# Performance work log

Hardware: AMD Instinct MI355X
Metric: run time of the kernel (lower is better)

Reference implementation:

```python
import jax, jax.numpy as jnp
import numpy as np

INF = 1e20


def setup_inputs() -> dict:
    key = jax.random.key(0)
    k1, k2, k3 = jax.random.split(key, 3)
    B, Q, M, F, D = 16, 64, 512, 16, 512
    return {
        "query_embed": jax.random.normal(k1, (B, Q, D), dtype=jnp.float32),
        "in_memory_embed": jax.random.normal(k2, (B, M, F, D), dtype=jnp.float32),
        "out_memory_embed": jax.random.normal(k3, (B, M, F, D), dtype=jnp.float32),
        "ctx_mask": jnp.ones((B, M, F), dtype=jnp.float32),
        "query_mask": jnp.ones((B, Q), dtype=jnp.float32),
    }


def reference(query_embed, in_memory_embed, out_memory_embed, ctx_mask, query_mask):
    # co-attention scores: [B, Q, M, F]
    attention = jnp.einsum("bqd,bmfd->bqmf", query_embed, in_memory_embed)
    # additive INF masking (torch: mask*att - (1-mask)*INF)
    cm = ctx_mask[:, None, :, :]            # [B,1,M,F]
    attention = cm * attention - (1.0 - cm) * INF
    qm = query_mask[:, :, None, None]       # [B,Q,1,1]
    attention = qm * attention - (1.0 - qm) * INF
    # NOTE: torch code computes a max-pool over Q for kb_feature_att but
    # immediately overwrites it with softmax of a ones/ctx mask -> dead code.
    mask = ctx_mask * 1.0 - (1.0 - ctx_mask) * INF        # [B,M,F]
    kb_feature_att = jax.nn.softmax(mask, axis=-1)        # [B,M,F]
    # weighted read over feature slots: [B,M,D]
    in_mem = jnp.einsum("bmf,bmfd->bmd", kb_feature_att, in_memory_embed)
    out_mem = out_memory_embed.sum(axis=2)                # [B,M,D]
    # max-pool over feature axis F -> [B,Q,M]
    att_qm = attention.max(axis=-1)
    probs = jax.nn.softmax(att_qm, axis=-1)               # over M
    new_query_embed = query_embed + jnp.einsum("bqm,bmd->bqd", probs, out_mem)
    probs2 = jax.nn.softmax(att_qm, axis=1)               # over Q
    in_mem = in_mem + jnp.einsum("bqm,bqd->bmd", probs2, new_query_embed)
    return (new_query_embed, in_mem, out_mem)
```

## Files before the change

### kernel.cpp

```cpp
#include <hip/hip_runtime.h>

#define INF_F 1e20f
#define B_ 16
#define Q_ 64
#define M_ 512
#define F_ 16
#define D_ 512

typedef __attribute__((ext_vector_type(8))) short short8v;
typedef __attribute__((ext_vector_type(4))) float f32x4;

static __device__ __forceinline__ float bits_f(unsigned u) { return __uint_as_float(u); }

static __device__ __forceinline__ void split4(float4 v, uint2& H, uint2& L) {
    unsigned hx = __float_as_uint(v.x) & 0xffff0000u, hy = __float_as_uint(v.y) & 0xffff0000u;
    unsigned hz = __float_as_uint(v.z) & 0xffff0000u, hw = __float_as_uint(v.w) & 0xffff0000u;
    H.x = (hx >> 16) | hy;
    H.y = (hz >> 16) | hw;
    L.x = (__float_as_uint(v.x - bits_f(hx)) >> 16) | (__float_as_uint(v.y - bits_f(hy)) & 0xffff0000u);
    L.y = (__float_as_uint(v.z - bits_f(hz)) >> 16) | (__float_as_uint(v.w - bits_f(hw)) & 0xffff0000u);
}

__global__ __launch_bounds__(256) void k_q_split(
    const float* __restrict__ q, short8v* __restrict__ qh, short8v* __restrict__ ql)
{
    int u = blockIdx.x * 256 + threadIdx.x;
    int row = u & 63, lg = (u >> 6) & 3, kc = (u >> 8) & 15, b = u >> 12;
    const float4* q4 = (const float4*)q;
    size_t s = (size_t)(b * 64 + row) * 128 + kc * 8 + lg * 2;
    float4 v0 = q4[s], v1 = q4[s + 1];
    uint2 H0, L0, H1, L1;
    split4(v0, H0, L0);
    split4(v1, H1, L1);
    *(uint4*)&qh[u] = make_uint4(H0.x, H0.y, H1.x, H1.y);
    *(uint4*)&ql[u] = make_uint4(L0.x, L0.y, L1.x, L1.y);
}

__global__ __launch_bounds__(256) void k_att_fused(
    const short8v* __restrict__ qhg, const short8v* __restrict__ qlg,
    const float* __restrict__ in_mem, const float* __restrict__ out_mem,
    const float* __restrict__ ctx_mask, const float* __restrict__ query_mask,
    float* __restrict__ att_qm, float* __restrict__ in_mem_base,
    float* __restrict__ out_mem_sum)
{
    __shared__ __align__(16) short Mh[5120];
    __shared__ __align__(16) short Ml[5120];

    const int bid = blockIdx.x;
    const int b   = bid & 15;
    const int m0  = (bid >> 4) * 8;
    const int t   = threadIdx.x;
    const int w   = t >> 6;
    const int lane = t & 63;
    const int lr  = lane & 15;
    const int lg  = lane >> 4;
    const int c   = lane & 7;
    const int b0  = (lane >> 3) & 1;
    const int mm  = 2 * w + b0;

    float wj[4];
    {
        const float* cm = ctx_mask + ((size_t)b * M_ + m0 + mm) * F_;
        float wv[16]; float mx = -INF_F;
        #pragma unroll
        for (int f = 0; f < 16; ++f) {
            float cv = cm[f];
            float v = cv - (1.0f - cv) * INF_F;
            wv[f] = v; mx = fmaxf(mx, v);
        }
        float s = 0.f;
        #pragma unroll
        for (int f = 0; f < 16; ++f) { wv[f] = __expf(wv[f] - mx); s += wv[f]; }
        float inv = 1.0f / s;
        #pragma unroll
        for (int i = 0; i < 4; ++i) wj[i] = wv[lg * 4 + i] * inv;
    }

    const float4* in4 = (const float4*)in_mem;
    const float4* ot4 = (const float4*)out_mem;
    const int grow  = ((b * M_ + m0 + mm) * F_ + lg * 4) * 128 + c;
    const int qb0   = b * 4096 + lg * 64 + lr;
    const int obase = (b * M_ + m0 + mm) * 128 + c;

    f32x4 acc[2][4];
    #pragma unroll
    for (int i = 0; i < 2; ++i)
        #pragma unroll
        for (int j = 0; j < 4; ++j) acc[i][j] = (f32x4){0, 0, 0, 0};

    float4 si[2][4], so[2][4];
    short8v qf[2][8];

    #pragma unroll
    for (int i = 0; i < 4; ++i) { si[0][i] = in4[grow + i * 128]; so[0][i] = ot4[grow + i * 128]; }
    #pragma unroll
    for (int tq = 0; tq < 4; ++tq) { qf[0][tq] = qhg[qb0 + tq * 16]; qf[0][4 + tq] = qlg[qb0 + tq * 16]; }

    #pragma unroll
    for (int kc = 0; kc < 16; ++kc) {
        const int cur = kc & 1, nxt = cur ^ 1;
        if (kc < 15) {
            const int go = grow + (kc + 1) * 8;
            #pragma unroll
            for (int i = 0; i < 4; ++i) { si[nxt][i] = in4[go + i * 128]; so[nxt][i] = ot4[go + i * 128]; }
            const int qb = qb0 + (kc + 1) * 256;
            #pragma unroll
            for (int tq = 0; tq < 4; ++tq) { qf[nxt][tq] = qhg[qb + tq * 16]; qf[nxt][4 + tq] = qlg[qb + tq * 16]; }
        }
        float4 sin_ = make_float4(0, 0, 0, 0), sot_ = make_float4(0, 0, 0, 0);
        #pragma unroll
        for (int i = 0; i < 4; ++i) {
            float4 a = si[cur][i];
            uint2 H, L; split4(a, H, L);
            const int rl = mm * 16 + lg * 4 + i;
            const int off = rl * 40 + (((c >> 1) ^ ((rl & 1) << 1)) << 3) + ((c & 1) << 2);
            *(uint2*)&Mh[off] = H;
            *(uint2*)&Ml[off] = L;
            sin_.x += wj[i] * a.x; sin_.y += wj[i] * a.y;
            sin_.z += wj[i] * a.z; sin_.w += wj[i] * a.w;
            float4 o = so[cur][i];
            sot_.x += o.x; sot_.y += o.y; sot_.z += o.z; sot_.w += o.w;
        }
        #pragma unroll
        for (int sh = 16; sh <= 32; sh <<= 1) {
            sin_.x += __shfl_xor(sin_.x, sh, 64); sin_.y += __shfl_xor(sin_.y, sh, 64);
            sin_.z += __shfl_xor(sin_.z, sh, 64); sin_.w += __shfl_xor(sin_.w, sh, 64);
            sot_.x += __shfl_xor(sot_.x, sh, 64); sot_.y += __shfl_xor(sot_.y, sh, 64);
            sot_.z += __shfl_xor(sot_.z, sh, 64); sot_.w += __shfl_xor(sot_.w, sh, 64);
        }
        if (lg == 0) {
            ((float4*)in_mem_base)[obase + kc * 8] = sin_;
            ((float4*)out_mem_sum)[obase + kc * 8] = sot_;
        }
        #pragma unroll
        for (int tm = 0; tm < 2; ++tm) {
            const int row = (2 * w + tm) * 16 + lr;
            const int off = row * 40 + ((lg ^ ((row & 1) << 1)) << 3);
            short8v bh = *(const short8v*)&Mh[off];
            short8v bl = *(const short8v*)&Ml[off];
            __builtin_amdgcn_s_setprio(1);
            #pragma unroll
            for (int tq = 0; tq < 4; ++tq) {
                short8v ah = qf[cur][tq], al = qf[cur][4 + tq];
                acc[tm][tq] = __builtin_amdgcn_mfma_f32_16x16x32_bf16(ah, bh, acc[tm][tq], 0, 0, 0);
                acc[tm][tq] = __builtin_amdgcn_mfma_f32_16x16x32_bf16(ah, bl, acc[tm][tq], 0, 0, 0);
                acc[tm][tq] = __builtin_amdgcn_mfma_f32_16x16x32_bf16(al, bh, acc[tm][tq], 0, 0, 0);
            }
            __builtin_amdgcn_s_setprio(0);
        }
    }

    #pragma unroll
    for (int tm = 0; tm < 2; ++tm) {
        int m = m0 + 2 * w + tm;
        float cmv = ctx_mask[((size_t)b * M_ + m) * F_ + lr];
        #pragma unroll
        for (int tq = 0; tq < 4; ++tq) {
            #pragma unroll
            for (int rg = 0; rg < 4; ++rg) {
                int q = tq * 16 + lg * 4 + rg;
                float qmv = query_mask[b * Q_ + q];
                float v = acc[tm][tq][rg];
                v = cmv * v - (1.0f - cmv) * INF_F;
                v = qmv * v - (1.0f - qmv) * INF_F;
                #pragma unroll
                for (int sh = 1; sh < 16; sh <<= 1) v = fmaxf(v, __shfl_xor(v, sh, 64));
                if (lr == 0)
                    att_qm[((size_t)b * Q_ + q) * M_ + m] = v;
            }
        }
    }
}

__global__ __launch_bounds__(128) void k_new_query(
    const float* __restrict__ att, const float* __restrict__ query,
    const float* __restrict__ out_sum, float* __restrict__ new_q)
{
    __shared__ float P[8][512];
    int bid = blockIdx.x;
    int b = bid & 15, qc = bid >> 4;
    int t = threadIdx.x;
    {
        int qi = t >> 4, l16 = t & 15;
        const float* row = att + ((size_t)b * Q_ + qc * 8 + qi) * M_;
        float vals[32]; float mx = -INF_F;
        #pragma unroll
        for (int i = 0; i < 32; ++i) { vals[i] = row[l16 + i * 16]; mx = fmaxf(mx, vals[i]); }
        #pragma unroll
        for (int s = 1; s < 16; s <<= 1) mx = fmaxf(mx, __shfl_xor(mx, s, 64));
        float sm = 0.f;
        #pragma unroll
        for (int i = 0; i < 32; ++i) { vals[i] = __expf(vals[i] - mx); sm += vals[i]; }
        #pragma unroll
        for (int s = 1; s < 16; s <<= 1) sm += __shfl_xor(sm, s, 64);
        float inv = 1.0f / sm;
        #pragma unroll
        for (int i = 0; i < 32; ++i) P[qi][l16 + i * 16] = vals[i] * inv;
    }
    __syncthreads();
    int c = t;
    const float4* o4 = (const float4*)out_sum + (size_t)b * M_ * 128 + c;
    const float4* q4 = (const float4*)query + ((size_t)b * Q_ + qc * 8) * 128 + c;
    float4 acc[8];
    #pragma unroll
    for (int qi = 0; qi < 8; ++qi) acc[qi] = q4[(size_t)qi * 128];
    for (int mm = 0; mm < M_; mm += 4) {
        float4 o0 = o4[(size_t)(mm + 0) * 128];
        float4 o1 = o4[(size_t)(mm + 1) * 128];
        float4 o2 = o4[(size_t)(mm + 2) * 128];
        float4 o3 = o4[(size_t)(mm + 3) * 128];
        #pragma unroll
        for (int qi = 0; qi < 8; ++qi) {
            float4 p = *(const float4*)&P[qi][mm];
            acc[qi].x += p.x * o0.x + p.y * o1.x + p.z * o2.x + p.w * o3.x;
            acc[qi].y += p.x * o0.y + p.y * o1.y + p.z * o2.y + p.w * o3.y;
            acc[qi].z += p.x * o0.z + p.y * o1.z + p.z * o2.z + p.w * o3.z;
            acc[qi].w += p.x * o0.w + p.y * o1.w + p.z * o2.w + p.w * o3.w;
        }
    }
    float4* n4 = (float4*)new_q + ((size_t)b * Q_ + qc * 8) * 128 + c;
    #pragma unroll
    for (int qi = 0; qi < 8; ++qi) n4[(size_t)qi * 128] = acc[qi];
}

__global__ __launch_bounds__(128) void k_in_mem(
    const float* __restrict__ att, const float* __restrict__ new_q,
    float* __restrict__ in_mem_io)
{
    __shared__ float P[8][64];
    int bid = blockIdx.x;
    int b = bid & 15, mc = bid >> 4;
    int m0 = mc * 8;
    int t = threadIdx.x;
    {
        int mi = t >> 4, l16 = t & 15;
        float v[4]; float mx = -INF_F;
        #pragma unroll
        for (int i = 0; i < 4; ++i) {
            v[i] = att[((size_t)b * Q_ + l16 + i * 16) * M_ + m0 + mi];
            mx = fmaxf(mx, v[i]);
        }
        #pragma unroll
        for (int s = 1; s < 16; s <<= 1) mx = fmaxf(mx, __shfl_xor(mx, s, 64));
        float sm = 0.f;
        #pragma unroll
        for (int i = 0; i < 4; ++i) { v[i] = __expf(v[i] - mx); sm += v[i]; }
        #pragma unroll
        for (int s = 1; s < 16; s <<= 1) sm += __shfl_xor(sm, s, 64);
        float inv = 1.0f / sm;
        #pragma unroll
        for (int i = 0; i < 4; ++i) P[mi][l16 + i * 16] = v[i] * inv;
    }
    __syncthreads();
    int c = t;
    float4* io = (float4*)in_mem_io + ((size_t)b * M_ + m0) * 128 + c;
    const float4* n4 = (const float4*)new_q + (size_t)b * Q_ * 128 + c;
    float4 acc[8];
    #pragma unroll
    for (int mi = 0; mi < 8; ++mi) acc[mi] = io[(size_t)mi * 128];
    for (int q = 0; q < Q_; q += 4) {
        float4 n0 = n4[(size_t)(q + 0) * 128];
        float4 n1 = n4[(size_t)(q + 1) * 128];
        float4 n2 = n4[(size_t)(q + 2) * 128];
        float4 n3 = n4[(size_t)(q + 3) * 128];
        #pragma unroll
        for (int mi = 0; mi < 8; ++mi) {
            float4 p = *(const float4*)&P[mi][q];
            acc[mi].x += p.x * n0.x + p.y * n1.x + p.z * n2.x + p.w * n3.x;
            acc[mi].y += p.x * n0.y + p.y * n1.y + p.z * n2.y + p.w * n3.y;
            acc[mi].z += p.x * n0.z + p.y * n1.z + p.z * n2.z + p.w * n3.z;
            acc[mi].w += p.x * n0.w + p.y * n1.w + p.z * n2.w + p.w * n3.w;
        }
    }
    #pragma unroll
    for (int mi = 0; mi < 8; ++mi) io[(size_t)mi * 128] = acc[mi];
}

extern "C" void kernel_launch(void* const* d_in, const int* in_sizes, int n_in,
                              void* d_out, int out_size, void* d_ws, size_t ws_size,
                              hipStream_t stream)
{
    const float* query      = (const float*)d_in[0];
    const float* in_mem     = (const float*)d_in[1];
    const float* out_mem    = (const float*)d_in[2];
    const float* ctx_mask   = (const float*)d_in[3];
    const float* query_mask = (const float*)d_in[4];

    float* out = (float*)d_out;
    float* new_q      = out;
    float* in_mem_out = out + (size_t)B_*Q_*D_;
    float* out_mem_o  = in_mem_out + (size_t)B_*M_*D_;

    float* ws       = (float*)d_ws;
    float* att_qm   = ws;
    short8v* qh     = (short8v*)(ws + (size_t)B_*Q_*M_);
    short8v* ql     = qh + 65536;

    hipLaunchKernelGGL(k_q_split, dim3(256), dim3(256), 0, stream, query, qh, ql);
    hipLaunchKernelGGL(k_att_fused, dim3((M_/8) * B_), dim3(256), 0, stream,
                       qh, ql, in_mem, out_mem, ctx_mask, query_mask,
                       att_qm, in_mem_out, out_mem_o);
    hipLaunchKernelGGL(k_new_query, dim3(8 * B_), dim3(128), 0, stream,
                       att_qm, query, out_mem_o, new_q);
    hipLaunchKernelGGL(k_in_mem, dim3(64 * B_), dim3(128), 0, stream,
                       att_qm, new_q, in_mem_out);
}
```

Before: 243.5 us.

## Restructure attention kernel with per-wave tiles and split out_mem sum blocks

The attention kernel now gives each wave 8 memory rows with 16 feature slots, so one wave holds a 64x128 tile and each Q fragment load is reused across eight MFMA tiles. Odd blocks handle the out_memory feature sum separately, which takes that streaming out of the MFMA blocks. The grid drops to 512 blocks under launch_bounds(256,1). The two downstream kernels also get larger per-block tiles (16 queries or 16 memory rows). Costs are higher register pressure (128 accumulator floats) and fewer blocks to hide memory latency, and the Q prefetch now sits after the MFMAs instead of being double-buffered.

New measurement: 280.9 us. 1.15x slower.

```diff
diff --git a/kernel.cpp b/kernel.cpp
--- a/kernel.cpp
+++ b/kernel.cpp
@@ -36,31 +36,51 @@
     *(uint4*)&ql[u] = make_uint4(L0.x, L0.y, L1.x, L1.y);
 }
 
-__global__ __launch_bounds__(256) void k_att_fused(
+__global__ __launch_bounds__(256, 1) void k_att(
     const short8v* __restrict__ qhg, const short8v* __restrict__ qlg,
     const float* __restrict__ in_mem, const float* __restrict__ out_mem,
     const float* __restrict__ ctx_mask, const float* __restrict__ query_mask,
     float* __restrict__ att_qm, float* __restrict__ in_mem_base,
     float* __restrict__ out_mem_sum)
 {
-    __shared__ __align__(16) short Mh[5120];
-    __shared__ __align__(16) short Ml[5120];
+    __shared__ __align__(16) short HB[4][4096];
+    __shared__ __align__(16) short LB[4][4096];
 
     const int bid = blockIdx.x;
-    const int b   = bid & 15;
-    const int m0  = (bid >> 4) * 8;
+    const int mg  = bid >> 1;
+    const int b   = mg >> 4;
+    const int m0  = (mg & 15) * 32;
     const int t   = threadIdx.x;
-    const int w   = t >> 6;
-    const int lane = t & 63;
-    const int lr  = lane & 15;
-    const int lg  = lane >> 4;
-    const int c   = lane & 7;
-    const int b0  = (lane >> 3) & 1;
-    const int mm  = 2 * w + b0;
-
-    float wj[4];
+
+    if (bid & 1) {
+        const int m = m0 + (t >> 3), c = t & 7;
+        const float4* src = (const float4*)out_mem + (size_t)((b * M_ + m) * F_) * 128;
+        float4* dst = (float4*)out_mem_sum + (size_t)(b * M_ + m) * 128;
+        #pragma unroll
+        for (int j = 0; j < 16; ++j) {
+            int col = c + j * 8;
+            float4 s = make_float4(0, 0, 0, 0);
+            #pragma unroll
+            for (int f = 0; f < 16; ++f) {
+                float4 v = src[f * 128 + col];
+                s.x += v.x; s.y += v.y; s.z += v.z; s.w += v.w;
+            }
+            dst[col] = s;
+        }
+        return;
+    }
+
+    const int w = t >> 6, lane = t & 63;
+    const int lr = lane & 15, lg = lane >> 4;
+    const int mm = lane >> 3, c = lane & 7;
+    const int mw0 = m0 + w * 8;
+    short* Hb = HB[w];
+    short* Lb = LB[w];
+    const int wg = (((c >> 1) ^ (mm & 3)) << 3) + ((c & 1) << 2);
+
+    float wj[16];
     {
-        const float* cm = ctx_mask + ((size_t)b * M_ + m0 + mm) * F_;
+        const float* cm = ctx_mask + (size_t)(b * M_ + mw0 + mm) * F_;
         float wv[16]; float mx = -INF_F;
         #pragma unroll
         for (int f = 0; f < 16; ++f) {
@@ -73,87 +93,88 @@
         for (int f = 0; f < 16; ++f) { wv[f] = __expf(wv[f] - mx); s += wv[f]; }
         float inv = 1.0f / s;
         #pragma unroll
-        for (int i = 0; i < 4; ++i) wj[i] = wv[lg * 4 + i] * inv;
+        for (int f = 0; f < 16; ++f) wj[f] = wv[f] * inv;
     }
 
     const float4* in4 = (const float4*)in_mem;
-    const float4* ot4 = (const float4*)out_mem;
-    const int grow  = ((b * M_ + m0 + mm) * F_ + lg * 4) * 128 + c;
-    const int qb0   = b * 4096 + lg * 64 + lr;
-    const int obase = (b * M_ + m0 + mm) * 128 + c;
-
-    f32x4 acc[2][4];
-    #pragma unroll
-    for (int i = 0; i < 2; ++i)
+    const size_t gbase = (size_t)((b * M_ + mw0 + mm) * F_) * 128 + c;
+    const size_t obase = (size_t)(b * M_ + mw0 + mm) * 128 + c;
+    const int qb0 = b * 4096 + lg * 64 + lr;
+
+    f32x4 acc[8][4];
+    #pragma unroll
+    for (int i = 0; i < 8; ++i)
         #pragma unroll
         for (int j = 0; j < 4; ++j) acc[i][j] = (f32x4){0, 0, 0, 0};
 
-    float4 si[2][4], so[2][4];
-    short8v qf[2][8];
-
-    #pragma unroll
-    for (int i = 0; i < 4; ++i) { si[0][i] = in4[grow + i * 128]; so[0][i] = ot4[grow + i * 128]; }
-    #pragma unroll
-    for (int tq = 0; tq < 4; ++tq) { qf[0][tq] = qhg[qb0 + tq * 16]; qf[0][4 + tq] = qlg[qb0 + tq * 16]; }
+    float4 sA[8], sB[8];
+    short8v qf[8];
+
+    #pragma unroll
+    for (int i = 0; i < 8; ++i) sA[i] = in4[gbase + (size_t)i * 128];
+    #pragma unroll
+    for (int i = 0; i < 8; ++i) sB[i] = in4[gbase + (size_t)(8 + i) * 128];
+    #pragma unroll
+    for (int tq = 0; tq < 4; ++tq) { qf[2*tq] = qhg[qb0 + tq*16]; qf[2*tq+1] = qlg[qb0 + tq*16]; }
 
     #pragma unroll
     for (int kc = 0; kc < 16; ++kc) {
-        const int cur = kc & 1, nxt = cur ^ 1;
+        float4 fs = make_float4(0, 0, 0, 0);
+        #pragma unroll
+        for (int i = 0; i < 8; ++i) {
+            float4 v = sA[i];
+            uint2 H, L; split4(v, H, L);
+            int woff = (mm * 16 + i) * 32 + wg;
+            *(uint2*)&Hb[woff] = H;
+            *(uint2*)&Lb[woff] = L;
+            fs.x += wj[i]*v.x; fs.y += wj[i]*v.y; fs.z += wj[i]*v.z; fs.w += wj[i]*v.w;
+        }
         if (kc < 15) {
-            const int go = grow + (kc + 1) * 8;
-            #pragma unroll
-            for (int i = 0; i < 4; ++i) { si[nxt][i] = in4[go + i * 128]; so[nxt][i] = ot4[go + i * 128]; }
-            const int qb = qb0 + (kc + 1) * 256;
-            #pragma unroll
-            for (int tq = 0; tq < 4; ++tq) { qf[nxt][tq] = qhg[qb + tq * 16]; qf[nxt][4 + tq] = qlg[qb + tq * 16]; }
-        }
-        float4 sin_ = make_float4(0, 0, 0, 0), sot_ = make_float4(0, 0, 0, 0);
-        #pragma unroll
-        for (int i = 0; i < 4; ++i) {
-            float4 a = si[cur][i];
-            uint2 H, L; split4(a, H, L);
-            const int rl = mm * 16 + lg * 4 + i;
-            const int off = rl * 40 + (((c >> 1) ^ ((rl & 1) << 1)) << 3) + ((c & 1) << 2);
-            *(uint2*)&Mh[off] = H;
-            *(uint2*)&Ml[off] = L;
-            sin_.x += wj[i] * a.x; sin_.y += wj[i] * a.y;
-            sin_.z += wj[i] * a.z; sin_.w += wj[i] * a.w;
-            float4 o = so[cur][i];
-            sot_.x += o.x; sot_.y += o.y; sot_.z += o.z; sot_.w += o.w;
-        }
-        #pragma unroll
-        for (int sh = 16; sh <= 32; sh <<= 1) {
-            sin_.x += __shfl_xor(sin_.x, sh, 64); sin_.y += __shfl_xor(sin_.y, sh, 64);
-            sin_.z += __shfl_xor(sin_.z, sh, 64); sin_.w += __shfl_xor(sin_.w, sh, 64);
-            sot_.x += __shfl_xor(sot_.x, sh, 64); sot_.y += __shfl_xor(sot_.y, sh, 64);
-            sot_.z += __shfl_xor(sot_.z, sh, 64); sot_.w += __shfl_xor(sot_.w, sh, 64);
-        }
-        if (lg == 0) {
-            ((float4*)in_mem_base)[obase + kc * 8] = sin_;
-            ((float4*)out_mem_sum)[obase + kc * 8] = sot_;
-        }
-        #pragma unroll
-        for (int tm = 0; tm < 2; ++tm) {
-            const int row = (2 * w + tm) * 16 + lr;
-            const int off = row * 40 + ((lg ^ ((row & 1) << 1)) << 3);
-            short8v bh = *(const short8v*)&Mh[off];
-            short8v bl = *(const short8v*)&Ml[off];
-            __builtin_amdgcn_s_setprio(1);
+            #pragma unroll
+            for (int i = 0; i < 8; ++i) sA[i] = in4[gbase + (size_t)i * 128 + (kc + 1) * 8];
+        }
+        #pragma unroll
+        for (int i = 0; i < 8; ++i) {
+            float4 v = sB[i];
+            uint2 H, L; split4(v, H, L);
+            int woff = (mm * 16 + 8 + i) * 32 + wg;
+            *(uint2*)&Hb[woff] = H;
+            *(uint2*)&Lb[woff] = L;
+            float wf = wj[8 + i];
+            fs.x += wf*v.x; fs.y += wf*v.y; fs.z += wf*v.z; fs.w += wf*v.w;
+        }
+        if (kc < 15) {
+            #pragma unroll
+            for (int i = 0; i < 8; ++i) sB[i] = in4[gbase + (size_t)(8 + i) * 128 + (kc + 1) * 8];
+        }
+        ((float4*)in_mem_base)[obase + kc * 8] = fs;
+
+        __builtin_amdgcn_s_setprio(1);
+        #pragma unroll
+        for (int tm = 0; tm < 8; ++tm) {
+            int roff = (tm * 16 + lr) * 32 + ((lg ^ (tm & 3)) << 3);
+            short8v bh = *(const short8v*)&Hb[roff];
+            short8v bl = *(const short8v*)&Lb[roff];
             #pragma unroll
             for (int tq = 0; tq < 4; ++tq) {
-                short8v ah = qf[cur][tq], al = qf[cur][4 + tq];
+                short8v ah = qf[2*tq], al = qf[2*tq+1];
                 acc[tm][tq] = __builtin_amdgcn_mfma_f32_16x16x32_bf16(ah, bh, acc[tm][tq], 0, 0, 0);
                 acc[tm][tq] = __builtin_amdgcn_mfma_f32_16x16x32_bf16(ah, bl, acc[tm][tq], 0, 0, 0);
                 acc[tm][tq] = __builtin_amdgcn_mfma_f32_16x16x32_bf16(al, bh, acc[tm][tq], 0, 0, 0);
             }
-            __builtin_amdgcn_s_setprio(0);
-        }
-    }
-
-    #pragma unroll
-    for (int tm = 0; tm < 2; ++tm) {
-        int m = m0 + 2 * w + tm;
-        float cmv = ctx_mask[((size_t)b * M_ + m) * F_ + lr];
+        }
+        __builtin_amdgcn_s_setprio(0);
+        if (kc < 15) {
+            int qb = qb0 + (kc + 1) * 256;
+            #pragma unroll
+            for (int tq = 0; tq < 4; ++tq) { qf[2*tq] = qhg[qb + tq*16]; qf[2*tq+1] = qlg[qb + tq*16]; }
+        }
+    }
+
+    #pragma unroll
+    for (int tm = 0; tm < 8; ++tm) {
+        int m = mw0 + tm;
+        float cmv = ctx_mask[(size_t)(b * M_ + m) * F_ + lr];
         #pragma unroll
         for (int tq = 0; tq < 4; ++tq) {
             #pragma unroll
@@ -166,23 +187,23 @@
                 #pragma unroll
                 for (int sh = 1; sh < 16; sh <<= 1) v = fmaxf(v, __shfl_xor(v, sh, 64));
                 if (lr == 0)
-                    att_qm[((size_t)b * Q_ + q) * M_ + m] = v;
+                    att_qm[(size_t)(b * Q_ + q) * M_ + m] = v;
             }
         }
     }
 }
 
-__global__ __launch_bounds__(128) void k_new_query(
+__global__ __launch_bounds__(256) void k_new_query(
     const float* __restrict__ att, const float* __restrict__ query,
     const float* __restrict__ out_sum, float* __restrict__ new_q)
 {
-    __shared__ float P[8][512];
+    __shared__ float P[16][512];
     int bid = blockIdx.x;
-    int b = bid & 15, qc = bid >> 4;
+    int b = bid >> 2, qc = bid & 3;
     int t = threadIdx.x;
     {
         int qi = t >> 4, l16 = t & 15;
-        const float* row = att + ((size_t)b * Q_ + qc * 8 + qi) * M_;
+        const float* row = att + (size_t)(b * Q_ + qc * 16 + qi) * M_;
         float vals[32]; float mx = -INF_F;
         #pragma unroll
         for (int i = 0; i < 32; ++i) { vals[i] = row[l16 + i * 16]; mx = fmaxf(mx, vals[i]); }
@@ -198,27 +219,27 @@
         for (int i = 0; i < 32; ++i) P[qi][l16 + i * 16] = vals[i] * inv;
     }
     __syncthreads();
-    int c = t;
-    const float4* o4 = (const float4*)out_sum + (size_t)b * M_ * 128 + c;
-    const float4* q4 = (const float4*)query + ((size_t)b * Q_ + qc * 8) * 128 + c;
+    int cph = t >> 7, cc = t & 127;
+    const float4* o4 = (const float4*)out_sum + (size_t)b * M_ * 128 + cc;
+    const float4* q4 = (const float4*)query + (size_t)(b * Q_ + qc * 16 + cph * 8) * 128 + cc;
     float4 acc[8];
     #pragma unroll
     for (int qi = 0; qi < 8; ++qi) acc[qi] = q4[(size_t)qi * 128];
-    for (int mm = 0; mm < M_; mm += 4) {
-        float4 o0 = o4[(size_t)(mm + 0) * 128];
-        float4 o1 = o4[(size_t)(mm + 1) * 128];
-        float4 o2 = o4[(size_t)(mm + 2) * 128];
-        float4 o3 = o4[(size_t)(mm + 3) * 128];
+    for (int mmv = 0; mmv < M_; mmv += 4) {
+        float4 o0 = o4[(size_t)(mmv + 0) * 128];
+        float4 o1 = o4[(size_t)(mmv + 1) * 128];
+        float4 o2 = o4[(size_t)(mmv + 2) * 128];
+        float4 o3 = o4[(size_t)(mmv + 3) * 128];
         #pragma unroll
         for (int qi = 0; qi < 8; ++qi) {
-            float4 p = *(const float4*)&P[qi][mm];
+            float4 p = *(const float4*)&P[cph * 8 + qi][mmv];
             acc[qi].x += p.x * o0.x + p.y * o1.x + p.z * o2.x + p.w * o3.x;
             acc[qi].y += p.x * o0.y + p.y * o1.y + p.z * o2.y + p.w * o3.y;
             acc[qi].z += p.x * o0.z + p.y * o1.z + p.z * o2.z + p.w * o3.z;
             acc[qi].w += p.x * o0.w + p.y * o1.w + p.z * o2.w + p.w * o3.w;
         }
     }
-    float4* n4 = (float4*)new_q + ((size_t)b * Q_ + qc * 8) * 128 + c;
+    float4* n4 = (float4*)new_q + (size_t)(b * Q_ + qc * 16 + cph * 8) * 128 + cc;
     #pragma unroll
     for (int qi = 0; qi < 8; ++qi) n4[(size_t)qi * 128] = acc[qi];
 }
@@ -227,53 +248,53 @@
     const float* __restrict__ att, const float* __restrict__ new_q,
     float* __restrict__ in_mem_io)
 {
-    __shared__ float P[8][64];
+    __shared__ float P[16][64];
     int bid = blockIdx.x;
     int b = bid & 15, mc = bid >> 4;
-    int m0 = mc * 8;
+    int m0 = mc * 16;
     int t = threadIdx.x;
     {
-        int mi = t >> 4, l16 = t & 15;
-        float v[4]; float mx = -INF_F;
-        #pragma unroll
-        for (int i = 0; i < 4; ++i) {
-            v[i] = att[((size_t)b * Q_ + l16 + i * 16) * M_ + m0 + mi];
+        int mi = t >> 3, l8 = t & 7;
+        float v[8]; float mx = -INF_F;
+        #pragma unroll
+        for (int i = 0; i < 8; ++i) {
+            v[i] = att[(size_t)(b * Q_ + l8 + i * 8) * M_ + m0 + mi];
             mx = fmaxf(mx, v[i]);
         }
         #pragma unroll
-        for (int s = 1; s < 16; s <<= 1) mx = fmaxf(mx, __shfl_xor(mx, s, 64));
+        for (int s = 1; s < 8; s <<= 1) mx = fmaxf(mx, __shfl_xor(mx, s, 64));
         float sm = 0.f;
         #pragma unroll
-        for (int i = 0; i < 4; ++i) { v[i] = __expf(v[i] - mx); sm += v[i]; }
-        #pragma unroll
-        for (int s = 1; s < 16; s <<= 1) sm += __shfl_xor(sm, s, 64);
+        for (int i = 0; i < 8; ++i) { v[i] = __expf(v[i] - mx); sm += v[i]; }
+        #pragma unroll
+        for (int s = 1; s < 8; s <<= 1) sm += __shfl_xor(sm, s, 64);
         float inv = 1.0f / sm;
         #pragma unroll
-        for (int i = 0; i < 4; ++i) P[mi][l16 + i * 16] = v[i] * inv;
+        for (int i = 0; i < 8; ++i) P[mi][l8 + i * 8] = v[i] * inv;
     }
     __syncthreads();
-    int c = t;
-    float4* io = (float4*)in_mem_io + ((size_t)b * M_ + m0) * 128 + c;
-    const float4* n4 = (const float4*)new_q + (size_t)b * Q_ * 128 + c;
-    float4 acc[8];
-    #pragma unroll
-    for (int mi = 0; mi < 8; ++mi) acc[mi] = io[(size_t)mi * 128];
-    for (int q = 0; q < Q_; q += 4) {
+    int cc = t;
+    float4* io = (float4*)in_mem_io + (size_t)(b * M_ + m0) * 128 + cc;
+    const float4* n4 = (const float4*)new_q + (size_t)b * Q_ * 128 + cc;
+    float4 acc[16];
+    #pragma unroll
+    for (int mi = 0; mi < 16; ++mi) acc[mi] = io[(size_t)mi * 128];
+    for (int q = 0; q < Q_; q += 2) {
         float4 n0 = n4[(size_t)(q + 0) * 128];
         float4 n1 = n4[(size_t)(q + 1) * 128];
-        float4 n2 = n4[(size_t)(q + 2) * 128];
-        float4 n3 = n4[(size_t)(q + 3) * 128];
-        #pragma unroll
-        for (int mi = 0; mi < 8; ++mi) {
-            float4 p = *(const float4*)&P[mi][q];
-            acc[mi].x += p.x * n0.x + p.y * n1.x + p.z * n2.x + p.w * n3.x;
-            acc[mi].y += p.x * n0.y + p.y * n1.y + p.z * n2.y + p.w * n3.y;
-            acc[mi].z += p.x * n0.z + p.y * n1.z + p.z * n2.z + p.w * n3.z;
-            acc[mi].w += p.x * n0.w + p.y * n1.w + p.z * n2.w + p.w * n3.w;
-        }
-    }
-    #pragma unroll
-    for (int mi = 0; mi < 8; ++mi) io[(size_t)mi * 128] = acc[mi];
+        #pragma unroll
+        for (int mi = 0; mi < 16; ++mi) {
+            float4 p2 = *(const float4*)&P[mi][q & 60];
+            float p0 = ((q & 2) == 0) ? p2.x : p2.z;
+            float p1 = ((q & 2) == 0) ? p2.y : p2.w;
+            acc[mi].x += p0 * n0.x + p1 * n1.x;
+            acc[mi].y += p0 * n0.y + p1 * n1.y;
+            acc[mi].z += p0 * n0.z + p1 * n1.z;
+            acc[mi].w += p0 * n0.w + p1 * n1.w;
+        }
+    }
+    #pragma unroll
+    for (int mi = 0; mi < 16; ++mi) io[(size_t)mi * 128] = acc[mi];
 }
 
 extern "C" void kernel_launch(void* const* d_in, const int* in_sizes, int n_in,
@@ -297,11 +318,11 @@
     short8v* ql     = qh + 65536;
 
     hipLaunchKernelGGL(k_q_split, dim3(256), dim3(256), 0, stream, query, qh, ql);
-    hipLaunchKernelGGL(k_att_fused, dim3((M_/8) * B_), dim3(256), 0, stream,
+    hipLaunchKernelGGL(k_att, dim3(512), dim3(256), 0, stream,
                        qh, ql, in_mem, out_mem, ctx_mask, query_mask,
                        att_qm, in_mem_out, out_mem_o);
-    hipLaunchKernelGGL(k_new_query, dim3(8 * B_), dim3(128), 0, stream,
+    hipLaunchKernelGGL(k_new_query, dim3(64), dim3(256), 0, stream,
                        att_qm, query, out_mem_o, new_q);
-    hipLaunchKernelGGL(k_in_mem, dim3(64 * B_), dim3(128), 0, stream,
+    hipLaunchKernelGGL(k_in_mem, dim3(32 * B_), dim3(128), 0, stream,
                        att_qm, new_q, in_mem_out);
 }
```

## Split out_mem reduction into separate block role and give each wave its own tile

Applied to the files above, without the earlier changes.

The fused attention kernel is restructured so that one in three blocks only sums out_memory_embed over F, while the other blocks handle the QK MFMA and the in_mem weighted read. Each wave now owns 4 memory rows with a private LDS tile that packs hi and lo bf16 halves together. The block-wide double-buffered prefetch is replaced by a single register buffer with prefetch interleaved around the MFMA loop, and occupancy is raised through launch bounds. The aim is to balance memory-bound and compute-bound work across CUs and to cut register pressure. The cost is a heterogeneous grid and less software pipelining of the q-fragment loads.

Measured after the change: 284.8 us. +17.0%, slower.

```diff
diff --git a/kernel.cpp b/kernel.cpp
--- a/kernel.cpp
+++ b/kernel.cpp
@@ -19,6 +19,12 @@
     H.y = (hz >> 16) | hw;
     L.x = (__float_as_uint(v.x - bits_f(hx)) >> 16) | (__float_as_uint(v.y - bits_f(hy)) & 0xffff0000u);
     L.y = (__float_as_uint(v.z - bits_f(hz)) >> 16) | (__float_as_uint(v.w - bits_f(hw)) & 0xffff0000u);
+}
+
+static __device__ __forceinline__ short8v mk8(uint2 a, uint2 b) {
+    union { uint4 u; short8v s; } r;
+    r.u = make_uint4(a.x, a.y, b.x, b.y);
+    return r.s;
 }
 
 __global__ __launch_bounds__(256) void k_q_split(
@@ -36,31 +42,53 @@
     *(uint4*)&ql[u] = make_uint4(L0.x, L0.y, L1.x, L1.y);
 }
 
-__global__ __launch_bounds__(256) void k_att_fused(
+__global__ __launch_bounds__(256, 3) void k_att(
     const short8v* __restrict__ qhg, const short8v* __restrict__ qlg,
     const float* __restrict__ in_mem, const float* __restrict__ out_mem,
     const float* __restrict__ ctx_mask, const float* __restrict__ query_mask,
     float* __restrict__ att_qm, float* __restrict__ in_mem_base,
     float* __restrict__ out_mem_sum)
 {
-    __shared__ __align__(16) short Mh[5120];
-    __shared__ __align__(16) short Ml[5120];
+    __shared__ __align__(16) uint4 SB[4][512];
 
     const int bid = blockIdx.x;
-    const int b   = bid & 15;
-    const int m0  = (bid >> 4) * 8;
-    const int t   = threadIdx.x;
-    const int w   = t >> 6;
-    const int lane = t & 63;
-    const int lr  = lane & 15;
-    const int lg  = lane >> 4;
-    const int c   = lane & 7;
-    const int b0  = (lane >> 3) & 1;
-    const int mm  = 2 * w + b0;
-
-    float wj[4];
+    const int u = bid / 3, r = bid - u * 3;
+    const int t = threadIdx.x;
+
+    if (r == 2) {
+        const int b = u >> 4;
+        const int m = (u & 15) * 32 + (t >> 3), c = t & 7;
+        const float4* src = (const float4*)out_mem + (size_t)((b * M_ + m) * F_) * 128;
+        float4* dst = (float4*)out_mem_sum + (size_t)(b * M_ + m) * 128;
+        #pragma unroll
+        for (int j = 0; j < 16; ++j) {
+            int col = c + j * 8;
+            float4 sv = make_float4(0, 0, 0, 0);
+            #pragma unroll
+            for (int f = 0; f < 16; ++f) {
+                float4 v = src[f * 128 + col];
+                sv.x += v.x; sv.y += v.y; sv.z += v.z; sv.w += v.w;
+            }
+            dst[col] = sv;
+        }
+        return;
+    }
+
+    const int k   = u * 2 + r;
+    const int b   = k >> 5;
+    const int m0  = (k & 31) * 16;
+    const int w   = t >> 6, lane = t & 63;
+    const int mw0 = m0 + w * 4;
+    const int mm = lane >> 4;
+    const int h  = (lane >> 3) & 1;
+    const int c  = lane & 7;
+    const int lr = lane & 15, lg = lane >> 4;
+
+    uint4* Wb = SB[w];
+
+    float wj[8];
     {
-        const float* cm = ctx_mask + ((size_t)b * M_ + m0 + mm) * F_;
+        const float* cm = ctx_mask + (size_t)(b * M_ + mw0 + mm) * F_;
         float wv[16]; float mx = -INF_F;
         #pragma unroll
         for (int f = 0; f < 16; ++f) {
@@ -73,87 +101,74 @@
         for (int f = 0; f < 16; ++f) { wv[f] = __expf(wv[f] - mx); s += wv[f]; }
         float inv = 1.0f / s;
         #pragma unroll
-        for (int i = 0; i < 4; ++i) wj[i] = wv[lg * 4 + i] * inv;
+        for (int i = 0; i < 8; ++i) wj[i] = wv[h * 8 + i] * inv;
     }
 
     const float4* in4 = (const float4*)in_mem;
-    const float4* ot4 = (const float4*)out_mem;
-    const int grow  = ((b * M_ + m0 + mm) * F_ + lg * 4) * 128 + c;
-    const int qb0   = b * 4096 + lg * 64 + lr;
-    const int obase = (b * M_ + m0 + mm) * 128 + c;
-
-    f32x4 acc[2][4];
-    #pragma unroll
-    for (int i = 0; i < 2; ++i)
+    const size_t gb = (size_t)((b * M_ + mw0 + mm) * F_ + h * 8) * 128 + c;
+    const size_t ob = (size_t)(b * M_ + mw0 + mm) * 128 + c;
+    const int qb0 = b * 4096 + lg * 64 + lr;
+
+    f32x4 acc[4][4];
+    #pragma unroll
+    for (int i = 0; i < 4; ++i)
         #pragma unroll
         for (int j = 0; j < 4; ++j) acc[i][j] = (f32x4){0, 0, 0, 0};
 
-    float4 si[2][4], so[2][4];
-    short8v qf[2][8];
-
-    #pragma unroll
-    for (int i = 0; i < 4; ++i) { si[0][i] = in4[grow + i * 128]; so[0][i] = ot4[grow + i * 128]; }
-    #pragma unroll
-    for (int tq = 0; tq < 4; ++tq) { qf[0][tq] = qhg[qb0 + tq * 16]; qf[0][4 + tq] = qlg[qb0 + tq * 16]; }
+    float4 si[8];
+    short8v qf[8];
+
+    #pragma unroll
+    for (int i = 0; i < 8; ++i) si[i] = in4[gb + (size_t)i * 128];
+    #pragma unroll
+    for (int tq = 0; tq < 4; ++tq) { qf[2*tq] = qhg[qb0 + tq*16]; qf[2*tq+1] = qlg[qb0 + tq*16]; }
 
     #pragma unroll
     for (int kc = 0; kc < 16; ++kc) {
-        const int cur = kc & 1, nxt = cur ^ 1;
+        float4 fs = make_float4(0, 0, 0, 0);
+        #pragma unroll
+        for (int i = 0; i < 8; ++i) {
+            float4 v = si[i];
+            uint2 H, L; split4(v, H, L);
+            int row = mm * 16 + h * 8 + i;
+            Wb[row * 8 + (c ^ (row & 7))] = make_uint4(H.x, H.y, L.x, L.y);
+            fs.x += wj[i]*v.x; fs.y += wj[i]*v.y; fs.z += wj[i]*v.z; fs.w += wj[i]*v.w;
+        }
+        fs.x += __shfl_xor(fs.x, 8, 64); fs.y += __shfl_xor(fs.y, 8, 64);
+        fs.z += __shfl_xor(fs.z, 8, 64); fs.w += __shfl_xor(fs.w, 8, 64);
+        if (h == 0) ((float4*)in_mem_base)[ob + kc * 8] = fs;
         if (kc < 15) {
-            const int go = grow + (kc + 1) * 8;
-            #pragma unroll
-            for (int i = 0; i < 4; ++i) { si[nxt][i] = in4[go + i * 128]; so[nxt][i] = ot4[go + i * 128]; }
-            const int qb = qb0 + (kc + 1) * 256;
-            #pragma unroll
-            for (int tq = 0; tq < 4; ++tq) { qf[nxt][tq] = qhg[qb + tq * 16]; qf[nxt][4 + tq] = qlg[qb + tq * 16]; }
-        }
-        float4 sin_ = make_float4(0, 0, 0, 0), sot_ = make_float4(0, 0, 0, 0);
-        #pragma unroll
-        for (int i = 0; i < 4; ++i) {
-            float4 a = si[cur][i];
-            uint2 H, L; split4(a, H, L);
-            const int rl = mm * 16 + lg * 4 + i;
-            const int off = rl * 40 + (((c >> 1) ^ ((rl & 1) << 1)) << 3) + ((c & 1) << 2);
-            *(uint2*)&Mh[off] = H;
-            *(uint2*)&Ml[off] = L;
-            sin_.x += wj[i] * a.x; sin_.y += wj[i] * a.y;
-            sin_.z += wj[i] * a.z; sin_.w += wj[i] * a.w;
-            float4 o = so[cur][i];
-            sot_.x += o.x; sot_.y += o.y; sot_.z += o.z; sot_.w += o.w;
-        }
-        #pragma unroll
-        for (int sh = 16; sh <= 32; sh <<= 1) {
-            sin_.x += __shfl_xor(sin_.x, sh, 64); sin_.y += __shfl_xor(sin_.y, sh, 64);
-            sin_.z += __shfl_xor(sin_.z, sh, 64); sin_.w += __shfl_xor(sin_.w, sh, 64);
-            sot_.x += __shfl_xor(sot_.x, sh, 64); sot_.y += __shfl_xor(sot_.y, sh, 64);
-            sot_.z += __shfl_xor(sot_.z, sh, 64); sot_.w += __shfl_xor(sot_.w, sh, 64);
-        }
-        if (lg == 0) {
-            ((float4*)in_mem_base)[obase + kc * 8] = sin_;
-            ((float4*)out_mem_sum)[obase + kc * 8] = sot_;
-        }
-        #pragma unroll
-        for (int tm = 0; tm < 2; ++tm) {
-            const int row = (2 * w + tm) * 16 + lr;
-            const int off = row * 40 + ((lg ^ ((row & 1) << 1)) << 3);
-            short8v bh = *(const short8v*)&Mh[off];
-            short8v bl = *(const short8v*)&Ml[off];
-            __builtin_amdgcn_s_setprio(1);
+            #pragma unroll
+            for (int i = 0; i < 8; ++i) si[i] = in4[gb + (size_t)i * 128 + (kc + 1) * 8];
+        }
+        __builtin_amdgcn_s_setprio(1);
+        #pragma unroll
+        for (int tm = 0; tm < 4; ++tm) {
+            int row = tm * 16 + lr;
+            uint4 s0 = Wb[row * 8 + ((lg * 2)     ^ (lr & 7))];
+            uint4 s1 = Wb[row * 8 + ((lg * 2 + 1) ^ (lr & 7))];
+            short8v bh = mk8(make_uint2(s0.x, s0.y), make_uint2(s1.x, s1.y));
+            short8v bl = mk8(make_uint2(s0.z, s0.w), make_uint2(s1.z, s1.w));
             #pragma unroll
             for (int tq = 0; tq < 4; ++tq) {
-                short8v ah = qf[cur][tq], al = qf[cur][4 + tq];
+                short8v ah = qf[2*tq], al = qf[2*tq+1];
                 acc[tm][tq] = __builtin_amdgcn_mfma_f32_16x16x32_bf16(ah, bh, acc[tm][tq], 0, 0, 0);
                 acc[tm][tq] = __builtin_amdgcn_mfma_f32_16x16x32_bf16(ah, bl, acc[tm][tq], 0, 0, 0);
                 acc[tm][tq] = __builtin_amdgcn_mfma_f32_16x16x32_bf16(al, bh, acc[tm][tq], 0, 0, 0);
             }
-            __builtin_amdgcn_s_setprio(0);
-        }
-    }
-
-    #pragma unroll
-    for (int tm = 0; tm < 2; ++tm) {
-        int m = m0 + 2 * w + tm;
-        float cmv = ctx_mask[((size_t)b * M_ + m) * F_ + lr];
+        }
+        __builtin_amdgcn_s_setprio(0);
+        if (kc < 15) {
+            int qb = qb0 + (kc + 1) * 256;
+            #pragma unroll
+            for (int tq = 0; tq < 4; ++tq) { qf[2*tq] = qhg[qb + tq*16]; qf[2*tq+1] = qlg[qb + tq*16]; }
+        }
+    }
+
+    #pragma unroll
+    for (int tm = 0; tm < 4; ++tm) {
+        int m = mw0 + tm;
+        float cmv = ctx_mask[(size_t)(b * M_ + m) * F_ + lr];
         #pragma unroll
         for (int tq = 0; tq < 4; ++tq) {
             #pragma unroll
@@ -166,7 +181,7 @@
                 #pragma unroll
                 for (int sh = 1; sh < 16; sh <<= 1) v = fmaxf(v, __shfl_xor(v, sh, 64));
                 if (lr == 0)
-                    att_qm[((size_t)b * Q_ + q) * M_ + m] = v;
+                    att_qm[(size_t)(b * Q_ + q) * M_ + m] = v;
             }
         }
     }
@@ -182,7 +197,7 @@
     int t = threadIdx.x;
     {
         int qi = t >> 4, l16 = t & 15;
-        const float* row = att + ((size_t)b * Q_ + qc * 8 + qi) * M_;
+        const float* row = att + (size_t)(b * Q_ + qc * 8 + qi) * M_;
         float vals[32]; float mx = -INF_F;
         #pragma unroll
         for (int i = 0; i < 32; ++i) { vals[i] = row[l16 + i * 16]; mx = fmaxf(mx, vals[i]); }
@@ -200,7 +215,7 @@
     __syncthreads();
     int c = t;
     const float4* o4 = (const float4*)out_sum + (size_t)b * M_ * 128 + c;
-    const float4* q4 = (const float4*)query + ((size_t)b * Q_ + qc * 8) * 128 + c;
+    const float4* q4 = (const float4*)query + (size_t)(b * Q_ + qc * 8) * 128 + c;
     float4 acc[8];
     #pragma unroll
     for (int qi = 0; qi < 8; ++qi) acc[qi] = q4[(size_t)qi * 128];
@@ -218,7 +233,7 @@
             acc[qi].w += p.x * o0.w + p.y * o1.w + p.z * o2.w + p.w * o3.w;
         }
     }
-    float4* n4 = (float4*)new_q + ((size_t)b * Q_ + qc * 8) * 128 + c;
+    float4* n4 = (float4*)new_q + (size_t)(b * Q_ + qc * 8) * 128 + c;
     #pragma unroll
     for (int qi = 0; qi < 8; ++qi) n4[(size_t)qi * 128] = acc[qi];
 }
@@ -237,7 +252,7 @@
         float v[4]; float mx = -INF_F;
         #pragma unroll
         for (int i = 0; i < 4; ++i) {
-            v[i] = att[((size_t)b * Q_ + l16 + i * 16) * M_ + m0 + mi];
+            v[i] = att[(size_t)(b * Q_ + l16 + i * 16) * M_ + m0 + mi];
             mx = fmaxf(mx, v[i]);
         }
         #pragma unroll
@@ -253,7 +268,7 @@
     }
     __syncthreads();
     int c = t;
-    float4* io = (float4*)in_mem_io + ((size_t)b * M_ + m0) * 128 + c;
+    float4* io = (float4*)in_mem_io + (size_t)(b * M_ + m0) * 128 + c;
     const float4* n4 = (const float4*)new_q + (size_t)b * Q_ * 128 + c;
     float4 acc[8];
     #pragma unroll
@@ -297,7 +312,7 @@
     short8v* ql     = qh + 65536;
 
     hipLaunchKernelGGL(k_q_split, dim3(256), dim3(256), 0, stream, query, qh, ql);
-    hipLaunchKernelGGL(k_att_fused, dim3((M_/8) * B_), dim3(256), 0, stream,
+    hipLaunchKernelGGL(k_att, dim3(768), dim3(256), 0, stream,
                        qh, ql, in_mem, out_mem, ctx_mask, query_mask,
                        att_qm, in_mem_out, out_mem_o);
     hipLaunchKernelGGL(k_new_query, dim3(8 * B_), dim3(128), 0, stream,
```
